# Optimization experiments

Hardware: AMD Instinct MI355X
Metric: run time of the kernel (lower is better)

## Reference

```python
import jax, jax.numpy as jnp
import numpy as np

EPS = 1e-6
N_HEADS = 6
N_POINTS = 4
B, LQ, C = 1, 96 * 96, 768


def _ln(x, w, b):
    mu = x.mean(-1, keepdims=True)
    var = ((x - mu) ** 2).mean(-1, keepdims=True)
    return (x - mu) * jax.lax.rsqrt(var + EPS) * w + b


def _corner(vbh, yi, xi, H, W):
    # vbh: [B, nH, H*W, Dh]; yi/xi: [B, nH, Lq, P] int32. Zero-padded OOB (grid_sample padding_mode='zeros').
    valid = (yi >= 0) & (yi < H) & (xi >= 0) & (xi < W)
    idx = jnp.clip(yi, 0, H - 1) * W + jnp.clip(xi, 0, W - 1)
    b, nh, lq, p = idx.shape
    g = jnp.take_along_axis(vbh, idx.reshape(b, nh, lq * p, 1), axis=2)
    g = g.reshape(b, nh, lq, p, vbh.shape[-1])
    return jnp.where(valid[..., None], g, jnp.zeros((), g.dtype))


def _msdeform(q, ref, feat, ss, so_w, so_b, aw_w, aw_b, vp_w, vp_b, op_w, op_b):
    # MSDeformAttn core: q [B,Lq,C], ref [B,Lq,L,2] in [0,1], feat [B,Len_in,C], ss np.int64 [L,2]=(H,W)
    b, lq, c = q.shape
    L = ss.shape[0]
    dh = c // N_HEADS
    value = (feat @ vp_w.T + vp_b).reshape(b, -1, N_HEADS, dh)
    offs = (q @ so_w.T + so_b).reshape(b, lq, N_HEADS, L, N_POINTS, 2)
    aw = jax.nn.softmax((q @ aw_w.T + aw_b).reshape(b, lq, N_HEADS, L * N_POINTS), -1)
    aw = aw.reshape(b, lq, N_HEADS, L, N_POINTS)
    # offset normalizer is (W, H) per level
    norm = jnp.asarray(np.ascontiguousarray(ss[:, ::-1]), dtype=q.dtype)  # [L,2]
    loc = ref[:, :, None, :, None, :] + offs / norm[None, None, None, :, None, :]
    out = jnp.zeros((b, N_HEADS, lq, dh), q.dtype)
    start = 0
    for l in range(L):
        H, W = int(ss[l, 0]), int(ss[l, 1])
        vbh = value[:, start:start + H * W].transpose(0, 2, 1, 3)  # [B,nH,H*W,Dh]
        # align_corners=False pixel coords: px = loc*W - 0.5
        px = loc[:, :, :, l, :, 0].transpose(0, 2, 1, 3) * W - 0.5  # [B,nH,Lq,P]
        py = loc[:, :, :, l, :, 1].transpose(0, 2, 1, 3) * H - 0.5
        x0 = jnp.floor(px).astype(jnp.int32)
        y0 = jnp.floor(py).astype(jnp.int32)
        fx = (px - x0)[..., None]
        fy = (py - y0)[..., None]
        samp = (_corner(vbh, y0, x0, H, W) * (1 - fy) * (1 - fx)
                + _corner(vbh, y0, x0 + 1, H, W) * (1 - fy) * fx
                + _corner(vbh, y0 + 1, x0, H, W) * fy * (1 - fx)
                + _corner(vbh, y0 + 1, x0 + 1, H, W) * fy * fx)  # [B,nH,Lq,P,Dh]
        w_l = aw[:, :, :, l, :].transpose(0, 2, 1, 3)[..., None]  # [B,nH,Lq,P,1]
        out = out + (samp * w_l).sum(3)
        start += H * W
    out = out.transpose(0, 2, 1, 3).reshape(b, lq, c)
    return out @ op_w.T + op_b


def setup_inputs() -> dict:
    key = jax.random.key(0)
    ks = jax.random.split(key, 14)
    lin = lambda k, o, i: 0.02 * jax.random.normal(k, (o, i), jnp.float32)
    return dict(
        query=jax.random.normal(ks[0], (B, LQ, C), jnp.float32),
        reference_points=jax.random.uniform(ks[1], (B, LQ, 1, 2), jnp.float32),
        feat=jax.random.normal(ks[2], (B, LQ, C), jnp.float32),
        feat_other_modalities=jax.random.normal(ks[3], (B, LQ, C), jnp.float32),
        spatial_shapes=np.array([[96, 96]], dtype=np.int64),
        level_start_index=np.array([0], dtype=np.int64),
        qn_w=jnp.ones(C), qn_b=jnp.zeros(C),
        fn_w=jnp.ones(C), fn_b=jnp.zeros(C),
        so_w=lin(ks[4], N_HEADS * N_POINTS * 2, C), so_b=0.02 * jax.random.normal(ks[12], (N_HEADS * N_POINTS * 2,), jnp.float32),
        aw_w=lin(ks[5], N_HEADS * N_POINTS, C), aw_b=jnp.zeros(N_HEADS * N_POINTS),
        vp_w=lin(ks[6], C, C), vp_b=jnp.zeros(C),
        op_w=lin(ks[7], C, C), op_b=jnp.zeros(C),
        gamma=0.02 * jax.random.normal(ks[8], (C,), jnp.float32),
        qn2_w=jnp.ones(C), qn2_b=jnp.zeros(C),
        fn2_w=jnp.ones(C), fn2_b=jnp.zeros(C),
        so2_w=lin(ks[9], N_HEADS * N_POINTS * 2, C), so2_b=0.02 * jax.random.normal(ks[13], (N_HEADS * N_POINTS * 2,), jnp.float32),
        aw2_w=lin(ks[10], N_HEADS * N_POINTS, C), aw2_b=jnp.zeros(N_HEADS * N_POINTS),
        vp2_w=lin(ks[11], C, C), vp2_b=jnp.zeros(C),
        op2_w=lin(jax.random.fold_in(key, 99), C, C), op2_b=jnp.zeros(C),
        gamma2=0.02 * jax.random.normal(jax.random.fold_in(key, 100), (C,), jnp.float32),
    )


def reference(query, reference_points, feat, feat_other_modalities, spatial_shapes, level_start_index,
              qn_w, qn_b, fn_w, fn_b, so_w, so_b, aw_w, aw_b, vp_w, vp_b, op_w, op_b, gamma,
              qn2_w, qn2_b, fn2_w, fn2_b, so2_w, so2_b, aw2_w, aw2_b, vp2_w, vp2_b, op2_w, op2_b, gamma2):
    ss = np.asarray(spatial_shapes)
    a = _msdeform(_ln(query, qn_w, qn_b), reference_points, _ln(feat, fn_w, fn_b), ss,
                  so_w, so_b, aw_w, aw_b, vp_w, vp_b, op_w, op_b)
    q = query + gamma * a
    a2 = _msdeform(_ln(q, qn2_w, qn2_b), reference_points,
                   _ln(feat_other_modalities, fn2_w, fn2_b), ss,
                   so2_w, so2_b, aw2_w, aw2_b, vp2_w, vp2_b, op2_w, op2_b)
    return q + gamma2 * a2
```

## Files before the change

### kernel.cpp

```cpp
#include <hip/hip_runtime.h>
#include <hip/hip_bf16.h>

typedef unsigned short u16;
typedef unsigned int u32;
typedef __attribute__((ext_vector_type(8))) short bf16x8;
typedef __attribute__((ext_vector_type(4))) float f32x4;
typedef __attribute__((ext_vector_type(4))) u32 u32x4;
typedef __attribute__((ext_vector_type(2))) u32 u32x2;

#define LQ 9216
#define CC 768
#define NH 6
#define DH 128
#define HH 96
#define WW 96

__device__ __forceinline__ u16 f2bf(float f) {
  union { float f; u32 u; } x; x.f = f;
  u32 r = x.u + 0x7fff + ((x.u >> 16) & 1);
  return (u16)(r >> 16);
}
__device__ __forceinline__ float u2f(u32 u) {
  union { u32 u; float f; } x; x.u = u; return x.f;
}

__device__ __forceinline__ void gl_lds16(const void* g, void* l) {
  __builtin_amdgcn_global_load_lds((const __attribute__((address_space(1))) void*)g,
                                   (__attribute__((address_space(3))) void*)l, 16, 0, 0);
}

__global__ __launch_bounds__(256)
void prep_weights(const float* __restrict__ vp, const float* __restrict__ op,
                  const float* __restrict__ vp2, const float* __restrict__ op2,
                  const float* __restrict__ so, const float* __restrict__ aw,
                  const float* __restrict__ so2, const float* __restrict__ aw2,
                  const float* __restrict__ so_b, const float* __restrict__ aw_b,
                  const float* __restrict__ so2_b, const float* __restrict__ aw2_b,
                  u16* __restrict__ w4, u16* __restrict__ cat1, u16* __restrict__ cat2,
                  float* __restrict__ b1, float* __restrict__ b2) {
  const int i = blockIdx.x * 256 + threadIdx.x;
  const int NW = 589824;
  if (i < 4 * NW) {
    const int m = i / NW, r = i - m * NW;
    const float* s = (m == 0) ? vp : (m == 1) ? op : (m == 2) ? vp2 : op2;
    w4[i] = f2bf(s[r]);
  } else if (i < 4 * NW + 2 * 98304) {
    const int j = i - 4 * NW;
    const int which = j / 98304;
    const int r = j - which * 98304;
    const int row = r / 768, colr = r - row * 768;
    float v = 0.f;
    if (row < 48) v = (which ? so2 : so)[row * 768 + colr];
    else if (row < 72) v = (which ? aw2 : aw)[(row - 48) * 768 + colr];
    (which ? cat2 : cat1)[r] = f2bf(v);
  } else if (i < 4 * NW + 2 * 98304 + 256) {
    const int j = i - 4 * NW - 2 * 98304;
    const int which = j >> 7, row = j & 127;
    float v = 0.f;
    if (row < 48) v = (which ? so2_b : so_b)[row];
    else if (row < 72) v = (which ? aw2_b : aw_b)[row - 48];
    (which ? b2 : b1)[row] = v;
  }
}

__device__ __forceinline__ void ln_wave_body(const float* __restrict__ x, const float* __restrict__ w,
                                             const float* __restrict__ b, u16* __restrict__ out, int row) {
  const int lane = threadIdx.x & 63;
  const float4* xr = (const float4*)(x + (size_t)row * CC);
  float4 v[3];
  #pragma unroll
  for (int j = 0; j < 3; ++j) v[j] = xr[lane + 64 * j];
  float s = 0.f, ss = 0.f;
  #pragma unroll
  for (int j = 0; j < 3; ++j) {
    s += v[j].x + v[j].y + v[j].z + v[j].w;
    ss += v[j].x * v[j].x + v[j].y * v[j].y + v[j].z * v[j].z + v[j].w * v[j].w;
  }
  #pragma unroll
  for (int o = 32; o > 0; o >>= 1) {
    s += __shfl_xor(s, o, 64);
    ss += __shfl_xor(ss, o, 64);
  }
  const float mu = s * (1.f / 768.f);
  const float var = ss * (1.f / 768.f) - mu * mu;
  const float rstd = rsqrtf(var + 1e-6f);
  const float4* wr = (const float4*)w;
  const float4* br = (const float4*)b;
  u32x2* orow = (u32x2*)(out + (size_t)row * CC);
  #pragma unroll
  for (int j = 0; j < 3; ++j) {
    const float4 wv = wr[lane + 64 * j];
    const float4 bv = br[lane + 64 * j];
    const float r0 = (v[j].x - mu) * rstd * wv.x + bv.x;
    const float r1 = (v[j].y - mu) * rstd * wv.y + bv.y;
    const float r2 = (v[j].z - mu) * rstd * wv.z + bv.z;
    const float r3 = (v[j].w - mu) * rstd * wv.w + bv.w;
    u32x2 o;
    o[0] = (u32)f2bf(r0) | ((u32)f2bf(r1) << 16);
    o[1] = (u32)f2bf(r2) | ((u32)f2bf(r3) << 16);
    orow[lane + 64 * j] = o;
  }
}

__global__ __launch_bounds__(256)
void ln_to_bf16(const float* __restrict__ x, const float* __restrict__ w,
                const float* __restrict__ b, u16* __restrict__ out) {
  const int row = blockIdx.x * 4 + (threadIdx.x >> 6);
  ln_wave_body(x, w, b, out, row);
}

__global__ __launch_bounds__(256)
void ln3_to_bf16(const float* __restrict__ x0, const float* __restrict__ w0, const float* __restrict__ b0, u16* __restrict__ o0,
                 const float* __restrict__ x1, const float* __restrict__ w1, const float* __restrict__ b1, u16* __restrict__ o1,
                 const float* __restrict__ x2, const float* __restrict__ w2, const float* __restrict__ b2, u16* __restrict__ o2) {
  const int sel = blockIdx.y;
  const float* x = (sel == 0) ? x0 : (sel == 1) ? x1 : x2;
  const float* w = (sel == 0) ? w0 : (sel == 1) ? w1 : w2;
  const float* b = (sel == 0) ? b0 : (sel == 1) ? b1 : b2;
  u16* o = (sel == 0) ? o0 : (sel == 1) ? o1 : o2;
  const int row = blockIdx.x * 4 + (threadIdx.x >> 6);
  ln_wave_body(x, w, b, o, row);
}

template <int TM, int MODE>
__device__ __forceinline__ void gemm_core(const u16* __restrict__ A, const u16* __restrict__ W,
                                          const float* __restrict__ bias, void* __restrict__ outv,
                                          const float* __restrict__ res, const float* __restrict__ gamma,
                                          int N, int K, int m0, int n0) {
  constexpr int FI = TM / 32;
  constexpr int NIA = TM / 32;
  __shared__ u16 As[TM * 64];
  __shared__ u16 Bs[64 * 64];
  const int tid = threadIdx.x;
  const int wv = tid >> 6, lane = tid & 63;
  const int quad = lane >> 4, l16 = lane & 15;
  const int wm = wv & 1, wn = wv >> 1;
  const int sr4 = lane >> 2;
  const int sc = (lane & 3) << 3;

  f32x4 acc[FI][2];
  #pragma unroll
  for (int i = 0; i < FI; ++i)
    #pragma unroll
    for (int j = 0; j < 2; ++j)
      acc[i][j] = (f32x4){0.f, 0.f, 0.f, 0.f};

  for (int k0 = 0; k0 < K; k0 += 64) {
    __syncthreads();
    #pragma unroll
    for (int j = 0; j < NIA; ++j) {
      const int g = wv * NIA + j;
      const int p = g & 1, rb = g >> 1;
      gl_lds16(A + (size_t)(m0 + rb * 16 + sr4) * K + (k0 + p * 32 + sc),
               (char*)As + p * (TM * 64) + rb * 1024 + lane * 16);
    }
    #pragma unroll
    for (int j = 0; j < 2; ++j) {
      const int g = wv * 2 + j;
      const int p = g & 1, rb = g >> 1;
      gl_lds16(W + (size_t)(n0 + rb * 16 + sr4) * K + (k0 + p * 32 + sc),
               (char*)Bs + p * 4096 + rb * 1024 + lane * 16);
    }
    __syncthreads();
    #pragma unroll
    for (int kk = 0; kk < 2; ++kk) {
      bf16x8 af[FI], bfr[2];
      #pragma unroll
      for (int i = 0; i < FI; ++i)
        af[i] = *(const bf16x8*)(As + kk * (TM * 32) + (wm * (TM / 2) + i * 16 + l16) * 32 + quad * 8);
      #pragma unroll
      for (int j = 0; j < 2; ++j)
        bfr[j] = *(const bf16x8*)(Bs + kk * 2048 + (wn * 32 + j * 16 + l16) * 32 + quad * 8);
      #pragma unroll
      for (int i = 0; i < FI; ++i)
        #pragma unroll
        for (int j = 0; j < 2; ++j)
          acc[i][j] = __builtin_amdgcn_mfma_f32_16x16x32_bf16(af[i], bfr[j], acc[i][j], 0, 0, 0);
    }
  }

  #pragma unroll
  for (int i = 0; i < FI; ++i) {
    #pragma unroll
    for (int j = 0; j < 2; ++j) {
      const int col = n0 + wn * 32 + j * 16 + l16;
      const float bs = bias[col];
      #pragma unroll
      for (int r = 0; r < 4; ++r) {
        const int row = m0 + wm * (TM / 2) + i * 16 + quad * 4 + r;
        const float v = acc[i][j][r] + bs;
        const size_t o = (size_t)row * N + col;
        if (MODE == 0) ((u16*)outv)[o] = f2bf(v);
        else if (MODE == 1) ((float*)outv)[o] = v;
        else ((float*)outv)[o] = res[o] + gamma[col] * v;
      }
    }
  }
}

template <int MODE>
__global__ __launch_bounds__(256, 5)
void gemm_bt(const u16* __restrict__ A, const u16* __restrict__ W,
             const float* __restrict__ bias, void* __restrict__ outv,
             const float* __restrict__ res, const float* __restrict__ gamma,
             int N, int K) {
  gemm_core<128, MODE>(A, W, bias, outv, res, gamma, N, K, blockIdx.x * 128, blockIdx.y * 64);
}

__global__ __launch_bounds__(256, 5)
void gemm_val_dual(const u16* __restrict__ A0, const u16* __restrict__ W0, const float* __restrict__ b0, u16* __restrict__ o0,
                   const u16* __restrict__ A1, const u16* __restrict__ W1, const float* __restrict__ b1, u16* __restrict__ o1,
                   int N, int K) {
  const int z = blockIdx.z;
  const u16* A = z ? A1 : A0;
  const u16* W = z ? W1 : W0;
  const float* b = z ? b1 : b0;
  u16* o = z ? o1 : o0;
  gemm_core<128, 0>(A, W, b, (void*)o, nullptr, nullptr, N, K, blockIdx.x * 128, blockIdx.y * 64);
}

__global__ __launch_bounds__(256, 5)
void gemm_small(const u16* __restrict__ A, const u16* __restrict__ W,
                const float* __restrict__ bias, float* __restrict__ out,
                int N, int K) {
  gemm_core<64, 1>(A, W, bias, (void*)out, nullptr, nullptr, N, K, blockIdx.x * 64, blockIdx.y * 64);
}

__global__ __launch_bounds__(256)
void msds_sample(const u16* __restrict__ value, const float* __restrict__ offaw,
                 const float* __restrict__ ref, u16* __restrict__ out) {
  const int t = blockIdx.x * 256 + threadIdx.x;
  const int pi = t >> 4;
  const int gl = t & 15;
  const int q = pi / NH;
  const int h = pi - q * NH;
  const float* oa = offaw + (size_t)q * 128;
  const float rx = ref[q * 2] * (float)WW - 0.5f;
  const float ry = ref[q * 2 + 1] * (float)HH - 0.5f;

  const float lg0 = oa[48 + h * 4 + 0], lg1 = oa[48 + h * 4 + 1];
  const float lg2 = oa[48 + h * 4 + 2], lg3 = oa[48 + h * 4 + 3];
  const float mx = fmaxf(fmaxf(lg0, lg1), fmaxf(lg2, lg3));
  const float e0 = __expf(lg0 - mx), e1 = __expf(lg1 - mx);
  const float e2 = __expf(lg2 - mx), e3 = __expf(lg3 - mx);
  const float inv = 1.f / (e0 + e1 + e2 + e3);
  const float wp[4] = {e0 * inv, e1 * inv, e2 * inv, e3 * inv};

  float acc[8];
  #pragma unroll
  for (int k = 0; k < 8; ++k) acc[k] = 0.f;

  const u16* vbase = value + h * DH + gl * 8;
  #pragma unroll
  for (int p = 0; p < 4; ++p) {
    const float px = rx + oa[h * 8 + p * 2];
    const float py = ry + oa[h * 8 + p * 2 + 1];
    const float fxf = floorf(px), fyf = floorf(py);
    const int x0 = (int)fxf, y0 = (int)fyf;
    const float fx = px - fxf, fy = py - fyf;
    const float cw[4] = {wp[p] * (1.f - fy) * (1.f - fx), wp[p] * (1.f - fy) * fx,
                         wp[p] * fy * (1.f - fx),         wp[p] * fy * fx};
    #pragma unroll
    for (int c = 0; c < 4; ++c) {
      const int yy = y0 + (c >> 1);
      const int xx = x0 + (c & 1);
      const bool valid = (yy >= 0) & (yy < HH) & (xx >= 0) & (xx < WW);
      const int yc = min(max(yy, 0), HH - 1);
      const int xc = min(max(xx, 0), WW - 1);
      const float w2 = valid ? cw[c] : 0.f;
      const u32x4 u = *(const u32x4*)(vbase + (size_t)(yc * WW + xc) * CC);
      #pragma unroll
      for (int k = 0; k < 4; ++k) {
        acc[2 * k]     += w2 * u2f(u[k] << 16);
        acc[2 * k + 1] += w2 * u2f(u[k] & 0xffff0000u);
      }
    }
  }
  u32x4 o;
  #pragma unroll
  for (int k = 0; k < 4; ++k)
    o[k] = (u32)f2bf(acc[2 * k]) | ((u32)f2bf(acc[2 * k + 1]) << 16);
  *(u32x4*)(out + (size_t)q * CC + h * DH + gl * 8) = o;
}

extern "C" void kernel_launch(void* const* d_in, const int* in_sizes, int n_in,
                              void* d_out, int out_size, void* d_ws, size_t ws_size,
                              hipStream_t stream) {
  const float* query = (const float*)d_in[0];
  const float* refp  = (const float*)d_in[1];
  const float* feat  = (const float*)d_in[2];
  const float* feat2 = (const float*)d_in[3];
  const float* qn_w = (const float*)d_in[6];
  const float* qn_b = (const float*)d_in[7];
  const float* fn_w = (const float*)d_in[8];
  const float* fn_b = (const float*)d_in[9];
  const float* so_w = (const float*)d_in[10];
  const float* so_b = (const float*)d_in[11];
  const float* aw_w = (const float*)d_in[12];
  const float* aw_b = (const float*)d_in[13];
  const float* vp_w = (const float*)d_in[14];
  const float* vp_b = (const float*)d_in[15];
  const float* op_w = (const float*)d_in[16];
  const float* op_b = (const float*)d_in[17];
  const float* gamma = (const float*)d_in[18];
  const float* qn2_w = (const float*)d_in[19];
  const float* qn2_b = (const float*)d_in[20];
  const float* fn2_w = (const float*)d_in[21];
  const float* fn2_b = (const float*)d_in[22];
  const float* so2_w = (const float*)d_in[23];
  const float* so2_b = (const float*)d_in[24];
  const float* aw2_w = (const float*)d_in[25];
  const float* aw2_b = (const float*)d_in[26];
  const float* vp2_w = (const float*)d_in[27];
  const float* vp2_b = (const float*)d_in[28];
  const float* op2_w = (const float*)d_in[29];
  const float* op2_b = (const float*)d_in[30];
  const float* gamma2 = (const float*)d_in[31];

  char* ws = (char*)d_ws;
  size_t off = 0;
  auto alloc = [&](size_t bytes) -> void* {
    void* p = ws + off;
    off += (bytes + 255) & ~(size_t)255;
    return p;
  };
  u16* w4    = (u16*)alloc((size_t)4 * 589824 * 2);
  u16* cat1  = (u16*)alloc((size_t)98304 * 2);
  u16* cat2  = (u16*)alloc((size_t)98304 * 2);
  float* b1  = (float*)alloc(128 * 4);
  float* b2  = (float*)alloc(128 * 4);
  u16* qn    = (u16*)alloc((size_t)LQ * CC * 2);
  u16* fn    = (u16*)alloc((size_t)LQ * CC * 2);
  u16* fn2   = (u16*)alloc((size_t)LQ * CC * 2);
  u16* val1  = (u16*)alloc((size_t)LQ * CC * 2);
  u16* val2  = (u16*)alloc((size_t)LQ * CC * 2);
  float* offaw = (float*)alloc((size_t)LQ * 128 * 4);
  float* qbuf  = (float*)alloc((size_t)LQ * CC * 4);

  dim3 blk(256);
  dim3 gbig(LQ / 128, CC / 64), gdual(LQ / 128, CC / 64, 2), gsm(LQ / 64, 2);

  prep_weights<<<9985, blk, 0, stream>>>(vp_w, op_w, vp2_w, op2_w, so_w, aw_w, so2_w, aw2_w,
                                         so_b, aw_b, so2_b, aw2_b, w4, cat1, cat2, b1, b2);
  ln3_to_bf16<<<dim3(LQ / 4, 3), blk, 0, stream>>>(query, qn_w, qn_b, qn,
                                                   feat, fn_w, fn_b, fn,
                                                   feat2, fn2_w, fn2_b, fn2);
  gemm_val_dual<<<gdual, blk, 0, stream>>>(fn, w4, vp_b, val1,
                                           fn2, w4 + 2 * 589824, vp2_b, val2, CC, CC);
  gemm_small<<<gsm, blk, 0, stream>>>(qn, cat1, b1, offaw, 128, CC);
  msds_sample<<<LQ * NH / 16, blk, 0, stream>>>(val1, offaw, refp, fn);
  gemm_bt<2><<<gbig, blk, 0, stream>>>(fn, w4 + 589824, op_b, (void*)qbuf, query, gamma, CC, CC);
  ln_to_bf16<<<LQ / 4, blk, 0, stream>>>(qbuf, qn2_w, qn2_b, qn);
  gemm_small<<<gsm, blk, 0, stream>>>(qn, cat2, b2, offaw, 128, CC);
  msds_sample<<<LQ * NH / 16, blk, 0, stream>>>(val2, offaw, refp, fn2);
  gemm_bt<2><<<gbig, blk, 0, stream>>>(fn2, w4 + 3 * 589824, op2_b, d_out, qbuf, gamma2, CC, CC);
}
```

Before: 333.9 us.

## Merge prep and LayerNorm launches, fuse value/offset GEMMs, store residual in bf16

```diff
diff --git a/kernel.cpp b/kernel.cpp
--- a/kernel.cpp
+++ b/kernel.cpp
@@ -23,44 +23,11 @@
 __device__ __forceinline__ float u2f(u32 u) {
   union { u32 u; float f; } x; x.u = u; return x.f;
 }
+__device__ __forceinline__ float bf2f(u16 u) { return u2f(((u32)u) << 16); }
 
 __device__ __forceinline__ void gl_lds16(const void* g, void* l) {
   __builtin_amdgcn_global_load_lds((const __attribute__((address_space(1))) void*)g,
                                    (__attribute__((address_space(3))) void*)l, 16, 0, 0);
-}
-
-__global__ __launch_bounds__(256)
-void prep_weights(const float* __restrict__ vp, const float* __restrict__ op,
-                  const float* __restrict__ vp2, const float* __restrict__ op2,
-                  const float* __restrict__ so, const float* __restrict__ aw,
-                  const float* __restrict__ so2, const float* __restrict__ aw2,
-                  const float* __restrict__ so_b, const float* __restrict__ aw_b,
-                  const float* __restrict__ so2_b, const float* __restrict__ aw2_b,
-                  u16* __restrict__ w4, u16* __restrict__ cat1, u16* __restrict__ cat2,
-                  float* __restrict__ b1, float* __restrict__ b2) {
-  const int i = blockIdx.x * 256 + threadIdx.x;
-  const int NW = 589824;
-  if (i < 4 * NW) {
-    const int m = i / NW, r = i - m * NW;
-    const float* s = (m == 0) ? vp : (m == 1) ? op : (m == 2) ? vp2 : op2;
-    w4[i] = f2bf(s[r]);
-  } else if (i < 4 * NW + 2 * 98304) {
-    const int j = i - 4 * NW;
-    const int which = j / 98304;
-    const int r = j - which * 98304;
-    const int row = r / 768, colr = r - row * 768;
-    float v = 0.f;
-    if (row < 48) v = (which ? so2 : so)[row * 768 + colr];
-    else if (row < 72) v = (which ? aw2 : aw)[(row - 48) * 768 + colr];
-    (which ? cat2 : cat1)[r] = f2bf(v);
-  } else if (i < 4 * NW + 2 * 98304 + 256) {
-    const int j = i - 4 * NW - 2 * 98304;
-    const int which = j >> 7, row = j & 127;
-    float v = 0.f;
-    if (row < 48) v = (which ? so2_b : so_b)[row];
-    else if (row < 72) v = (which ? aw2_b : aw_b)[row - 48];
-    (which ? b2 : b1)[row] = v;
-  }
 }
 
 __device__ __forceinline__ void ln_wave_body(const float* __restrict__ x, const float* __restrict__ w,
@@ -102,35 +69,110 @@
   }
 }
 
+#define NPREP 9985
 __global__ __launch_bounds__(256)
-void ln_to_bf16(const float* __restrict__ x, const float* __restrict__ w,
-                const float* __restrict__ b, u16* __restrict__ out) {
+void prelude(const float* __restrict__ vp, const float* __restrict__ op,
+             const float* __restrict__ vp2, const float* __restrict__ op2,
+             const float* __restrict__ so, const float* __restrict__ aw,
+             const float* __restrict__ so2, const float* __restrict__ aw2,
+             const float* __restrict__ so_b, const float* __restrict__ aw_b,
+             const float* __restrict__ so2_b, const float* __restrict__ aw2_b,
+             u16* __restrict__ w4, u16* __restrict__ cat1, u16* __restrict__ cat2,
+             float* __restrict__ b1, float* __restrict__ b2,
+             const float* __restrict__ x0, const float* __restrict__ w0, const float* __restrict__ bb0, u16* __restrict__ o0,
+             const float* __restrict__ x1, const float* __restrict__ w1, const float* __restrict__ bb1, u16* __restrict__ o1,
+             const float* __restrict__ x2, const float* __restrict__ w2, const float* __restrict__ bb2, u16* __restrict__ o2) {
+  const int blk = blockIdx.x;
+  if (blk < NPREP) {
+    const int i = blk * 256 + threadIdx.x;
+    const int NW = 589824;
+    if (i < 4 * NW) {
+      const int m = i / NW, r = i - m * NW;
+      const float* s = (m == 0) ? vp : (m == 1) ? op : (m == 2) ? vp2 : op2;
+      w4[i] = f2bf(s[r]);
+    } else if (i < 4 * NW + 2 * 98304) {
+      const int j = i - 4 * NW;
+      const int which = j / 98304;
+      const int r = j - which * 98304;
+      const int row = r / 768, colr = r - row * 768;
+      float v = 0.f;
+      if (row < 48) v = (which ? so2 : so)[row * 768 + colr];
+      else if (row < 72) v = (which ? aw2 : aw)[(row - 48) * 768 + colr];
+      (which ? cat2 : cat1)[r] = f2bf(v);
+    } else if (i < 4 * NW + 2 * 98304 + 256) {
+      const int j = i - 4 * NW - 2 * 98304;
+      const int which = j >> 7, row = j & 127;
+      float v = 0.f;
+      if (row < 48) v = (which ? so2_b : so_b)[row];
+      else if (row < 72) v = (which ? aw2_b : aw_b)[row - 48];
+      (which ? b2 : b1)[row] = v;
+    }
+  } else {
+    const int r = blk - NPREP;
+    const int sel = r / (LQ / 4);
+    const int row = (r - sel * (LQ / 4)) * 4 + (threadIdx.x >> 6);
+    const float* x = (sel == 0) ? x0 : (sel == 1) ? x1 : x2;
+    const float* w = (sel == 0) ? w0 : (sel == 1) ? w1 : w2;
+    const float* b = (sel == 0) ? bb0 : (sel == 1) ? bb1 : bb2;
+    u16* o = (sel == 0) ? o0 : (sel == 1) ? o1 : o2;
+    ln_wave_body(x, w, b, o, row);
+  }
+}
+
+__global__ __launch_bounds__(256)
+void ln_bf16_to_bf16(const u16* __restrict__ x, const float* __restrict__ w,
+                     const float* __restrict__ b, u16* __restrict__ out) {
   const int row = blockIdx.x * 4 + (threadIdx.x >> 6);
-  ln_wave_body(x, w, b, out, row);
-}
-
-__global__ __launch_bounds__(256)
-void ln3_to_bf16(const float* __restrict__ x0, const float* __restrict__ w0, const float* __restrict__ b0, u16* __restrict__ o0,
-                 const float* __restrict__ x1, const float* __restrict__ w1, const float* __restrict__ b1, u16* __restrict__ o1,
-                 const float* __restrict__ x2, const float* __restrict__ w2, const float* __restrict__ b2, u16* __restrict__ o2) {
-  const int sel = blockIdx.y;
-  const float* x = (sel == 0) ? x0 : (sel == 1) ? x1 : x2;
-  const float* w = (sel == 0) ? w0 : (sel == 1) ? w1 : w2;
-  const float* b = (sel == 0) ? b0 : (sel == 1) ? b1 : b2;
-  u16* o = (sel == 0) ? o0 : (sel == 1) ? o1 : o2;
-  const int row = blockIdx.x * 4 + (threadIdx.x >> 6);
-  ln_wave_body(x, w, b, o, row);
+  const int lane = threadIdx.x & 63;
+  const u32x2* xr = (const u32x2*)(x + (size_t)row * CC);
+  float v[3][4];
+  #pragma unroll
+  for (int j = 0; j < 3; ++j) {
+    const u32x2 u = xr[lane + 64 * j];
+    v[j][0] = u2f(u[0] << 16);
+    v[j][1] = u2f(u[0] & 0xffff0000u);
+    v[j][2] = u2f(u[1] << 16);
+    v[j][3] = u2f(u[1] & 0xffff0000u);
+  }
+  float s = 0.f, ss = 0.f;
+  #pragma unroll
+  for (int j = 0; j < 3; ++j)
+    #pragma unroll
+    for (int k = 0; k < 4; ++k) { s += v[j][k]; ss += v[j][k] * v[j][k]; }
+  #pragma unroll
+  for (int o = 32; o > 0; o >>= 1) {
+    s += __shfl_xor(s, o, 64);
+    ss += __shfl_xor(ss, o, 64);
+  }
+  const float mu = s * (1.f / 768.f);
+  const float var = ss * (1.f / 768.f) - mu * mu;
+  const float rstd = rsqrtf(var + 1e-6f);
+  const float4* wr = (const float4*)w;
+  const float4* br = (const float4*)b;
+  u32x2* orow = (u32x2*)(out + (size_t)row * CC);
+  #pragma unroll
+  for (int j = 0; j < 3; ++j) {
+    const float4 wv = wr[lane + 64 * j];
+    const float4 bv = br[lane + 64 * j];
+    u32x2 o;
+    const float r0 = (v[j][0] - mu) * rstd * wv.x + bv.x;
+    const float r1 = (v[j][1] - mu) * rstd * wv.y + bv.y;
+    const float r2 = (v[j][2] - mu) * rstd * wv.z + bv.z;
+    const float r3 = (v[j][3] - mu) * rstd * wv.w + bv.w;
+    o[0] = (u32)f2bf(r0) | ((u32)f2bf(r1) << 16);
+    o[1] = (u32)f2bf(r2) | ((u32)f2bf(r3) << 16);
+    orow[lane + 64 * j] = o;
+  }
 }
 
 template <int TM, int MODE>
-__device__ __forceinline__ void gemm_core(const u16* __restrict__ A, const u16* __restrict__ W,
+__device__ __forceinline__ void gemm_core(u16* __restrict__ As, u16* __restrict__ Bs,
+                                          const u16* __restrict__ A, const u16* __restrict__ W,
                                           const float* __restrict__ bias, void* __restrict__ outv,
-                                          const float* __restrict__ res, const float* __restrict__ gamma,
+                                          const void* __restrict__ res, const float* __restrict__ gamma,
                                           int N, int K, int m0, int n0) {
   constexpr int FI = TM / 32;
   constexpr int NIA = TM / 32;
-  __shared__ u16 As[TM * 64];
-  __shared__ u16 Bs[64 * 64];
   const int tid = threadIdx.x;
   const int wv = tid >> 6, lane = tid & 63;
   const int quad = lane >> 4, l16 = lane & 15;
@@ -192,9 +234,29 @@
         const size_t o = (size_t)row * N + col;
         if (MODE == 0) ((u16*)outv)[o] = f2bf(v);
         else if (MODE == 1) ((float*)outv)[o] = v;
-        else ((float*)outv)[o] = res[o] + gamma[col] * v;
+        else if (MODE == 2) ((u16*)outv)[o] = f2bf(((const float*)res)[o] + gamma[col] * v);
+        else ((float*)outv)[o] = bf2f(((const u16*)res)[o]) + gamma[col] * v;
       }
     }
+  }
+}
+
+__global__ __launch_bounds__(256, 5)
+void gemm_fused1(const u16* __restrict__ fn, const u16* __restrict__ wv1, const float* __restrict__ vb1, u16* __restrict__ val1,
+                 const u16* __restrict__ fn2, const u16* __restrict__ wv2, const float* __restrict__ vb2, u16* __restrict__ val2,
+                 const u16* __restrict__ qn, const u16* __restrict__ cat1, const float* __restrict__ b1, float* __restrict__ offaw) {
+  __shared__ u16 As[128 * 64];
+  __shared__ u16 Bs[64 * 64];
+  const int id = blockIdx.x;
+  if (id < 1728) {
+    const int z = id / 864, rem = id - z * 864;
+    const int x = rem % 72, y = rem / 72;
+    gemm_core<128, 0>(As, Bs, z ? fn2 : fn, z ? wv2 : wv1, z ? vb2 : vb1,
+                      (void*)(z ? val2 : val1), nullptr, nullptr, CC, CC, x * 128, y * 64);
+  } else {
+    const int sid = id - 1728;
+    const int x = sid % 144, y = sid / 144;
+    gemm_core<64, 1>(As, Bs, qn, cat1, b1, (void*)offaw, nullptr, nullptr, 128, CC, x * 64, y * 64);
   }
 }
 
@@ -202,28 +264,20 @@
 __global__ __launch_bounds__(256, 5)
 void gemm_bt(const u16* __restrict__ A, const u16* __restrict__ W,
              const float* __restrict__ bias, void* __restrict__ outv,
-             const float* __restrict__ res, const float* __restrict__ gamma,
+             const void* __restrict__ res, const float* __restrict__ gamma,
              int N, int K) {
-  gemm_core<128, MODE>(A, W, bias, outv, res, gamma, N, K, blockIdx.x * 128, blockIdx.y * 64);
-}
-
-__global__ __launch_bounds__(256, 5)
-void gemm_val_dual(const u16* __restrict__ A0, const u16* __restrict__ W0, const float* __restrict__ b0, u16* __restrict__ o0,
-                   const u16* __restrict__ A1, const u16* __restrict__ W1, const float* __restrict__ b1, u16* __restrict__ o1,
-                   int N, int K) {
-  const int z = blockIdx.z;
-  const u16* A = z ? A1 : A0;
-  const u16* W = z ? W1 : W0;
-  const float* b = z ? b1 : b0;
-  u16* o = z ? o1 : o0;
-  gemm_core<128, 0>(A, W, b, (void*)o, nullptr, nullptr, N, K, blockIdx.x * 128, blockIdx.y * 64);
+  __shared__ u16 As[128 * 64];
+  __shared__ u16 Bs[64 * 64];
+  gemm_core<128, MODE>(As, Bs, A, W, bias, outv, res, gamma, N, K, blockIdx.x * 128, blockIdx.y * 64);
 }
 
 __global__ __launch_bounds__(256, 5)
 void gemm_small(const u16* __restrict__ A, const u16* __restrict__ W,
                 const float* __restrict__ bias, float* __restrict__ out,
                 int N, int K) {
-  gemm_core<64, 1>(A, W, bias, (void*)out, nullptr, nullptr, N, K, blockIdx.x * 64, blockIdx.y * 64);
+  __shared__ u16 As[64 * 64];
+  __shared__ u16 Bs[64 * 64];
+  gemm_core<64, 1>(As, Bs, A, W, bias, (void*)out, nullptr, nullptr, N, K, blockIdx.x * 64, blockIdx.y * 64);
 }
 
 __global__ __launch_bounds__(256)
@@ -234,17 +288,21 @@
   const int gl = t & 15;
   const int q = pi / NH;
   const int h = pi - q * NH;
-  const float* oa = offaw + (size_t)q * 128;
-  const float rx = ref[q * 2] * (float)WW - 0.5f;
-  const float ry = ref[q * 2 + 1] * (float)HH - 0.5f;
-
-  const float lg0 = oa[48 + h * 4 + 0], lg1 = oa[48 + h * 4 + 1];
-  const float lg2 = oa[48 + h * 4 + 2], lg3 = oa[48 + h * 4 + 3];
-  const float mx = fmaxf(fmaxf(lg0, lg1), fmaxf(lg2, lg3));
-  const float e0 = __expf(lg0 - mx), e1 = __expf(lg1 - mx);
-  const float e2 = __expf(lg2 - mx), e3 = __expf(lg3 - mx);
+  const float4* oaf = (const float4*)(offaw + (size_t)q * 128);
+  const float4 of0 = oaf[h * 2];
+  const float4 of1 = oaf[h * 2 + 1];
+  const float4 lg = oaf[12 + h];
+  const float2 rp = ((const float2*)ref)[q];
+  const float rx = rp.x * (float)WW - 0.5f;
+  const float ry = rp.y * (float)HH - 0.5f;
+
+  const float mx = fmaxf(fmaxf(lg.x, lg.y), fmaxf(lg.z, lg.w));
+  const float e0 = __expf(lg.x - mx), e1 = __expf(lg.y - mx);
+  const float e2 = __expf(lg.z - mx), e3 = __expf(lg.w - mx);
   const float inv = 1.f / (e0 + e1 + e2 + e3);
   const float wp[4] = {e0 * inv, e1 * inv, e2 * inv, e3 * inv};
+  const float ox[4] = {of0.x, of0.z, of1.x, of1.z};
+  const float oy[4] = {of0.y, of0.w, of1.y, of1.w};
 
   float acc[8];
   #pragma unroll
@@ -253,8 +311,8 @@
   const u16* vbase = value + h * DH + gl * 8;
   #pragma unroll
   for (int p = 0; p < 4; ++p) {
-    const float px = rx + oa[h * 8 + p * 2];
-    const float py = ry + oa[h * 8 + p * 2 + 1];
+    const float px = rx + ox[p];
+    const float py = ry + oy[p];
     const float fxf = floorf(px), fyf = floorf(py);
     const int x0 = (int)fxf, y0 = (int)fyf;
     const float fx = px - fxf, fy = py - fyf;
@@ -335,23 +393,24 @@
   u16* val1  = (u16*)alloc((size_t)LQ * CC * 2);
   u16* val2  = (u16*)alloc((size_t)LQ * CC * 2);
   float* offaw = (float*)alloc((size_t)LQ * 128 * 4);
-  float* qbuf  = (float*)alloc((size_t)LQ * CC * 4);
+  u16* qbuf  = (u16*)alloc((size_t)LQ * CC * 2);
 
   dim3 blk(256);
-  dim3 gbig(LQ / 128, CC / 64), gdual(LQ / 128, CC / 64, 2), gsm(LQ / 64, 2);
-
-  prep_weights<<<9985, blk, 0, stream>>>(vp_w, op_w, vp2_w, op2_w, so_w, aw_w, so2_w, aw2_w,
-                                         so_b, aw_b, so2_b, aw2_b, w4, cat1, cat2, b1, b2);
-  ln3_to_bf16<<<dim3(LQ / 4, 3), blk, 0, stream>>>(query, qn_w, qn_b, qn,
-                                                   feat, fn_w, fn_b, fn,
-                                                   feat2, fn2_w, fn2_b, fn2);
-  gemm_val_dual<<<gdual, blk, 0, stream>>>(fn, w4, vp_b, val1,
-                                           fn2, w4 + 2 * 589824, vp2_b, val2, CC, CC);
-  gemm_small<<<gsm, blk, 0, stream>>>(qn, cat1, b1, offaw, 128, CC);
+  dim3 gbig(LQ / 128, CC / 64), gsm(LQ / 64, 2);
+
+  prelude<<<NPREP + 3 * (LQ / 4), blk, 0, stream>>>(
+      vp_w, op_w, vp2_w, op2_w, so_w, aw_w, so2_w, aw2_w,
+      so_b, aw_b, so2_b, aw2_b, w4, cat1, cat2, b1, b2,
+      query, qn_w, qn_b, qn,
+      feat, fn_w, fn_b, fn,
+      feat2, fn2_w, fn2_b, fn2);
+  gemm_fused1<<<2016, blk, 0, stream>>>(fn, w4, vp_b, val1,
+                                        fn2, w4 + 2 * 589824, vp2_b, val2,
+                                        qn, cat1, b1, offaw);
   msds_sample<<<LQ * NH / 16, blk, 0, stream>>>(val1, offaw, refp, fn);
   gemm_bt<2><<<gbig, blk, 0, stream>>>(fn, w4 + 589824, op_b, (void*)qbuf, query, gamma, CC, CC);
-  ln_to_bf16<<<LQ / 4, blk, 0, stream>>>(qbuf, qn2_w, qn2_b, qn);
+  ln_bf16_to_bf16<<<LQ / 4, blk, 0, stream>>>(qbuf, qn2_w, qn2_b, qn);
   gemm_small<<<gsm, blk, 0, stream>>>(qn, cat2, b2, offaw, 128, CC);
   msds_sample<<<LQ * NH / 16, blk, 0, stream>>>(val2, offaw, refp, fn2);
-  gemm_bt<2><<<gbig, blk, 0, stream>>>(fn2, w4 + 3 * 589824, op2_b, d_out, qbuf, gamma2, CC, CC);
-}
+  gemm_bt<3><<<gbig, blk, 0, stream>>>(fn2, w4 + 3 * 589824, op2_b, d_out, qbuf, gamma2, CC, CC);
+}
```

Result: faster. 318.8 us (-4.5%).
